# Kernel tuning notes

Measured on AMD Instinct MI355X. Metric: run time of the kernel, lower is better.

## Reference

```python
import jax, jax.numpy as jnp
import numpy as np

B, S, E = 2, 4096, 640
H, D, G = 4, 256, 1      # n_heads, head_dim, n_kv_groups
WINDOW = 512
SCALING = 256.0 ** -0.5  # query_pre_attn_scalar ** -0.5
EPS = 1e-6


def rmsnorm(x, scale):
    # Gemma variant: weight = 1 + scale, computed in fp32 over last dim
    xf = x.astype(jnp.float32)
    var = jnp.mean(xf * xf, axis=-1, keepdims=True)
    return (xf * jax.lax.rsqrt(var + EPS) * (1.0 + scale.astype(jnp.float32))).astype(x.dtype)


def apply_rope(x, cos, sin):
    # x: [B, h, S, D]; cos/sin: [S, D]
    half = x.shape[-1] // 2
    x1, x2 = x[..., :half], x[..., half:]
    rotated = jnp.concatenate([-x2, x1], axis=-1)
    return (x * cos[None, None] + rotated * sin[None, None]).astype(x.dtype)


def setup_inputs() -> dict:
    key = jax.random.key(0)
    ks = jax.random.split(key, 6)
    x = jax.random.normal(ks[0], (B, S, E), dtype=jnp.float32)
    # weights (torch Linear weight.T layout: [in, out])
    Wq = jax.random.normal(ks[1], (E, H * D), dtype=jnp.float32) * 0.02
    Wk = jax.random.normal(ks[2], (E, G * D), dtype=jnp.float32) * 0.02
    Wv = jax.random.normal(ks[3], (E, G * D), dtype=jnp.float32) * 0.02
    Wo = jax.random.normal(ks[4], (H * D, E), dtype=jnp.float32) * 0.02
    q_scale = jnp.zeros((D,), dtype=jnp.float32)
    k_scale = jnp.zeros((D,), dtype=jnp.float32)
    # RoPE tables (theta = rope_local_base = 10000 for sliding layers)
    inv_freq = 1.0 / (10000.0 ** (jnp.arange(0, D, 2, dtype=jnp.float32) / D))
    angles = jnp.arange(S, dtype=jnp.float32)[:, None] * inv_freq[None, :]
    angles = jnp.concatenate([angles, angles], axis=1)  # [S, D]
    cos, sin = jnp.cos(angles), jnp.sin(angles)
    # causal + sliding-window mask; True = masked out
    i = jnp.arange(S)[:, None]
    j = jnp.arange(S)[None, :]
    mask = (j > i) | ((i - j) >= WINDOW)
    return {"x": x, "mask": mask, "cos": cos, "sin": sin,
            "Wq": Wq, "Wk": Wk, "Wv": Wv, "Wo": Wo,
            "q_scale": q_scale, "k_scale": k_scale}


def reference(x, mask, cos, sin, Wq, Wk, Wv, Wo, q_scale, k_scale):
    b, s, _ = x.shape
    q = (x @ Wq).reshape(b, s, H, D).transpose(0, 2, 1, 3)  # [B,H,S,D]
    k = (x @ Wk).reshape(b, s, G, D).transpose(0, 2, 1, 3)  # [B,G,S,D]
    v = (x @ Wv).reshape(b, s, G, D).transpose(0, 2, 1, 3)  # [B,G,S,D]
    q = rmsnorm(q, q_scale)
    k = rmsnorm(k, k_scale)
    q = apply_rope(q, cos, sin)
    k = apply_rope(k, cos, sin)
    # GQA: K/V have G=1 heads; broadcasting replaces repeat_interleave
    scores = (q * SCALING) @ jnp.swapaxes(k, -1, -2)  # [B,H,S,S]
    scores = jnp.where(mask[None, None], -jnp.inf, scores)
    attn = jax.nn.softmax(scores, axis=-1)
    out = attn @ v                                     # [B,H,S,D]
    out = out.transpose(0, 2, 1, 3).reshape(b, s, H * D)
    return out @ Wo
```

## Files before the change

### kernel.cpp

```cpp
#include <hip/hip_runtime.h>
#include <hip/hip_bf16.h>
#include <stdint.h>

#define BB 2
#define SS 4096
#define EE 640
#define HH 4
#define DD 256
#define WIN 512

typedef __attribute__((ext_vector_type(8))) short bv8;
typedef __attribute__((ext_vector_type(4))) float fv4;
typedef __attribute__((ext_vector_type(16))) float fv16;

__device__ __forceinline__ unsigned short f2b(float f) {
  union { float f; unsigned u; } a; a.f = f;
  unsigned r = a.u + 0x7fffu + ((a.u >> 16) & 1u);
  return (unsigned short)(r >> 16);
}
__device__ __forceinline__ float b2f(unsigned short s) {
  union { unsigned u; float f; } a; a.u = ((unsigned)s) << 16;
  return a.f;
}
__device__ __forceinline__ unsigned pk2(float lo, float hi_) {
  return (unsigned)f2b(lo) | ((unsigned)f2b(hi_) << 16);
}

typedef const __attribute__((address_space(1))) unsigned int* as1u;
typedef __attribute__((address_space(3))) unsigned int* as3u;
__device__ __forceinline__ void gld16(const unsigned short* g, unsigned short* l) {
  __builtin_amdgcn_global_load_lds((as1u)(const void*)g, (as3u)(void*)l, 16, 0, 0);
}

__global__ __launch_bounds__(256) void k_cast_bf16(const float* __restrict__ src,
                                                   unsigned short* __restrict__ dst, int n4) {
  int i = blockIdx.x * 256 + threadIdx.x;
  if (i >= n4) return;
  fv4 v = ((const fv4*)src)[i];
  ushort4 o; o.x = f2b(v.x); o.y = f2b(v.y); o.z = f2b(v.z); o.w = f2b(v.w);
  ((ushort4*)dst)[i] = o;
}

__global__ __launch_bounds__(256) void k_wtrans(const float* __restrict__ Wq,
    const float* __restrict__ Wk, const float* __restrict__ Wv,
    const float* __restrict__ Wo, unsigned short* __restrict__ wqkv,
    unsigned short* __restrict__ wo) {
  __shared__ float tile[32][33];
  const int z = blockIdx.z, bx = blockIdx.x, by = blockIdx.y;
  const float* src; unsigned short* dst; int ss, ds;
  if (z == 0)      { if (bx >= 20 || by >= 32) return; src = Wq; dst = wqkv;              ss = 1024; ds = 640; }
  else if (z == 1) { if (bx >= 20 || by >= 8)  return; src = Wk; dst = wqkv + 1024 * 640; ss = 256;  ds = 640; }
  else if (z == 2) { if (bx >= 20 || by >= 8)  return; src = Wv; dst = wqkv + 1280 * 640; ss = 256;  ds = 640; }
  else             { if (bx >= 32 || by >= 20) return; src = Wo; dst = wo;                ss = 640;  ds = 1024; }
  int r0 = bx * 32, c0 = by * 32;
  int t = threadIdx.x;
  int rr = t >> 3, cc = (t & 7) * 4;
  fv4 x = *(const fv4*)(src + (size_t)(r0 + rr) * ss + c0 + cc);
#pragma unroll
  for (int i = 0; i < 4; ++i) tile[cc + i][rr] = x[i];
  __syncthreads();
  ushort4 o;
  o.x = f2b(tile[rr][cc + 0]); o.y = f2b(tile[rr][cc + 1]);
  o.z = f2b(tile[rr][cc + 2]); o.w = f2b(tile[rr][cc + 3]);
  *(ushort4*)(dst + (size_t)(c0 + rr) * ds + r0 + cc) = o;
}

__global__ __launch_bounds__(256) void k_gemm_qkv(const unsigned short* __restrict__ A,
    const unsigned short* __restrict__ Bt,
    const float* __restrict__ cosp, const float* __restrict__ sinp,
    const float* __restrict__ qsc, const float* __restrict__ ksc,
    unsigned short* __restrict__ qo, unsigned short* __restrict__ ko,
    unsigned short* __restrict__ vt) {
  __shared__ __align__(16) char shl[40960];
  unsigned short* la = (unsigned short*)shl;
  unsigned short* lb = (unsigned short*)(shl + 8192);
  const int K = EE;
  const int bid = blockIdx.x;
  const int gidx = (bid & 7) * 96 + (bid >> 3);
  const int mt = gidx / 6, nt = gidx % 6;
  const int m0 = mt * 64, n0 = nt * 256;
  const int tid = threadIdx.x, lane = tid & 63, wave = tid >> 6;
  const int g = lane >> 4, lr = lane & 15;
  const int wm = (wave >> 1) * 32, wn = (wave & 1) * 128;
  fv4 acc[2][8] = {};
  const unsigned short* ga0 = A + (size_t)(m0 + (tid >> 2)) * K + (tid & 3) * 8;
  const unsigned short* gb0 = Bt + (size_t)(n0 + (tid >> 2)) * K + (tid & 3) * 8;
  auto stage = [&](int k0, int pp) {
    gld16(ga0 + k0, la + pp * 2048 + wave * 512);
#pragma unroll
    for (int c = 0; c < 4; ++c)
      gld16(gb0 + (size_t)(c * 64) * K + k0, lb + pp * 8192 + (c * 64 + wave * 16) * 32);
  };
  stage(0, 0);
  const int NIT = K >> 5;
  for (int it = 0; it < NIT; ++it) {
    const int p = it & 1;
    if (it > 0) __builtin_amdgcn_s_barrier();
    if (it + 1 < NIT) {
      stage((it + 1) * 32, p ^ 1);
      asm volatile("s_waitcnt vmcnt(5)" ::: "memory");
    } else {
      asm volatile("s_waitcnt vmcnt(0)" ::: "memory");
    }
    __builtin_amdgcn_sched_barrier(0);
    __builtin_amdgcn_s_barrier();
    bv8 af[2], bf[8];
#pragma unroll
    for (int mi = 0; mi < 2; ++mi)
      af[mi] = *(const bv8*)(la + p * 2048 + (wm + mi * 16 + lr) * 32 + g * 8);
#pragma unroll
    for (int ni = 0; ni < 8; ++ni)
      bf[ni] = *(const bv8*)(lb + p * 8192 + (wn + ni * 16 + lr) * 32 + g * 8);
    __builtin_amdgcn_s_setprio(1);
#pragma unroll
    for (int mi = 0; mi < 2; ++mi)
#pragma unroll
      for (int ni = 0; ni < 8; ++ni)
        acc[mi][ni] = __builtin_amdgcn_mfma_f32_16x16x32_bf16(af[mi], bf[ni], acc[mi][ni], 0, 0, 0);
    __builtin_amdgcn_s_setprio(0);
  }
  __syncthreads();
  unsigned short* cw = (unsigned short*)shl;
  float* rsum = (float*)(shl + 33792);
#pragma unroll
  for (int mi = 0; mi < 2; ++mi)
#pragma unroll
    for (int r = 0; r < 4; ++r) {
      int row = wm + mi * 16 + g * 4 + r;
#pragma unroll
      for (int ni = 0; ni < 8; ++ni)
        cw[row * 264 + wn + ni * 16 + lr] = f2b(acc[mi][ni][r]);
    }
  __syncthreads();
  const int m = m0 + (tid & 63);
  const int b = m >> 12, s = m & 4095;
  if (nt < 5) {
    const int qq = tid >> 6;
    const int row = tid & 63;
    const int dlo = qq * 32, dhi = dlo + 128;
    float xlo[32], xhi[32];
    float ss2 = 0.f;
#pragma unroll
    for (int j8 = 0; j8 < 4; ++j8) {
      bv8 v0 = *(const bv8*)(cw + row * 264 + dlo + j8 * 8);
      bv8 v1 = *(const bv8*)(cw + row * 264 + dhi + j8 * 8);
#pragma unroll
      for (int e = 0; e < 8; ++e) {
        float a0 = b2f((unsigned short)v0[e]);
        float a1 = b2f((unsigned short)v1[e]);
        xlo[j8 * 8 + e] = a0; xhi[j8 * 8 + e] = a1;
        ss2 += a0 * a0 + a1 * a1;
      }
    }
    rsum[row * 4 + qq] = ss2;
    __syncthreads();
    float tot = rsum[row * 4 + 0] + rsum[row * 4 + 1] + rsum[row * 4 + 2] + rsum[row * 4 + 3];
    float rs = rsqrtf(tot * (1.0f / 256.0f) + 1e-6f);
    const float* scp = (nt < 4) ? qsc : ksc;
    const float mult = (nt < 4) ? (0.0625f * 1.44269504f) : 1.0f;
    unsigned short* dst = (nt < 4)
        ? qo + ((size_t)(b * HH + nt) * SS + s) * 256
        : ko + ((size_t)b * SS + s) * 256;
    const float* crow = cosp + (size_t)s * 256;
    const float* srow = sinp + (size_t)s * 256;
#pragma unroll
    for (int j4 = 0; j4 < 8; ++j4) {
      fv4 sclo = *(const fv4*)(scp + dlo + j4 * 4);
      fv4 schi = *(const fv4*)(scp + dhi + j4 * 4);
      fv4 clo = *(const fv4*)(crow + dlo + j4 * 4);
      fv4 chi = *(const fv4*)(crow + dhi + j4 * 4);
      fv4 slo = *(const fv4*)(srow + dlo + j4 * 4);
      fv4 shi = *(const fv4*)(srow + dhi + j4 * 4);
      ushort4 olo, ohi;
#pragma unroll
      for (int e = 0; e < 4; ++e) {
        float nlo = xlo[j4 * 4 + e] * rs * (1.0f + sclo[e]);
        float nhi = xhi[j4 * 4 + e] * rs * (1.0f + schi[e]);
        float rlo = (nlo * clo[e] - nhi * slo[e]) * mult;
        float rhi = (nhi * chi[e] + nlo * shi[e]) * mult;
        ((unsigned short*)&olo)[e] = f2b(rlo);
        ((unsigned short*)&ohi)[e] = f2b(rhi);
      }
      *(ushort4*)(dst + dlo + j4 * 4) = olo;
      *(ushort4*)(dst + dhi + j4 * 4) = ohi;
    }
  } else {
    const int d = tid;
    const int bb2 = (m0 >> 12), s0 = m0 & 4095;
    ushort4 buf[16];
#pragma unroll
    for (int r4 = 0; r4 < 16; ++r4) {
      ushort4 o;
      o.x = cw[(r4 * 4 + 0) * 264 + d];
      o.y = cw[(r4 * 4 + 1) * 264 + d];
      o.z = cw[(r4 * 4 + 2) * 264 + d];
      o.w = cw[(r4 * 4 + 3) * 264 + d];
      buf[r4] = o;
    }
    unsigned short* dst = vt + ((size_t)bb2 * 256 + d) * SS + s0;
#pragma unroll
    for (int r4 = 0; r4 < 16; ++r4) *(ushort4*)(dst + r4 * 4) = buf[r4];
  }
}

template <bool OUT_BF16, int BN>
__global__ __launch_bounds__(256) void k_gemm(const unsigned short* __restrict__ A,
    const unsigned short* __restrict__ Bt, void* __restrict__ Cp,
    int M, int N, int K, int nt_n) {
  __shared__ unsigned short la[2][128 * 32];
  __shared__ unsigned short lb[2][BN * 32];
  const int bid = blockIdx.x;
  const int gidx = (bid & 7) * (gridDim.x >> 3) + (bid >> 3);
  const int m0 = (gidx / nt_n) * 128, n0 = (gidx % nt_n) * BN;
  const int tid = threadIdx.x, lane = tid & 63, wave = tid >> 6;
  const int g = lane >> 4, lr = lane & 15;
  constexpr int MI = (BN == 128) ? 4 : 2;
  const int wm = (BN == 128) ? (wave >> 1) * 64 : wave * 32;
  const int wn = (BN == 128) ? (wave & 1) * 64 : 0;
  fv4 acc[MI][4] = {};
  const int srow = wave * 32 + (lane >> 2);
  const int sch = (lane & 3) * 8;
  const unsigned short* ga0 = A + (size_t)(m0 + srow) * K + sch;
  const int srowb = (BN == 128) ? srow : (wave * 16 + (lane >> 2));
  const unsigned short* gb0 = Bt + (size_t)(n0 + srowb) * K + sch;
  const int NIT = K >> 5;
  auto stage = [&](int k0, int pp) {
    unsigned short* lad = la[pp] + wave * 1024;
    unsigned short* lbd = lb[pp] + ((BN == 128) ? wave * 1024 : wave * 512);
    gld16(ga0 + k0, lad);
    gld16(ga0 + (size_t)16 * K + k0, lad + 512);
    gld16(gb0 + k0, lbd);
    if constexpr (BN == 128) gld16(gb0 + (size_t)16 * K + k0, lbd + 512);
  };
  stage(0, 0);
  for (int it = 0; it < NIT; ++it) {
    const int p = it & 1;
    if (it > 0) __builtin_amdgcn_s_barrier();
    if (it + 1 < NIT) {
      stage((it + 1) * 32, p ^ 1);
      if constexpr (BN == 128)
        asm volatile("s_waitcnt vmcnt(4)" ::: "memory");
      else
        asm volatile("s_waitcnt vmcnt(3)" ::: "memory");
    } else {
      asm volatile("s_waitcnt vmcnt(0)" ::: "memory");
    }
    __builtin_amdgcn_sched_barrier(0);
    __builtin_amdgcn_s_barrier();
    bv8 af[MI], bf[4];
#pragma unroll
    for (int mi = 0; mi < MI; ++mi)
      af[mi] = *(const bv8*)(la[p] + (wm + mi * 16 + lr) * 32 + g * 8);
#pragma unroll
    for (int ni = 0; ni < 4; ++ni)
      bf[ni] = *(const bv8*)(lb[p] + (wn + ni * 16 + lr) * 32 + g * 8);
    __builtin_amdgcn_s_setprio(1);
#pragma unroll
    for (int mi = 0; mi < MI; ++mi)
#pragma unroll
      for (int ni = 0; ni < 4; ++ni)
        acc[mi][ni] = __builtin_amdgcn_mfma_f32_16x16x32_bf16(af[mi], bf[ni], acc[mi][ni], 0, 0, 0);
    __builtin_amdgcn_s_setprio(0);
  }
#pragma unroll
  for (int mi = 0; mi < MI; ++mi) {
#pragma unroll
    for (int r = 0; r < 4; ++r) {
      size_t row = (size_t)(m0 + wm + mi * 16 + g * 4 + r);
#pragma unroll
      for (int ni = 0; ni < 4; ++ni) {
        int col = n0 + wn + ni * 16 + lr;
        float val = acc[mi][ni][r];
        if constexpr (OUT_BF16)
          ((unsigned short*)Cp)[row * N + col] = f2b(val);
        else
          ((float*)Cp)[row * N + col] = val;
      }
    }
  }
}

__global__ __launch_bounds__(512, 2) void k_attn(const unsigned short* __restrict__ q,
    const unsigned short* __restrict__ kg, const unsigned short* __restrict__ vtg,
    unsigned short* __restrict__ att) {
  __shared__ __align__(16) char ldsbuf[133120];
  __shared__ float lsb[4][32];
  unsigned short* kt = (unsigned short*)ldsbuf;
  unsigned short* vl = (unsigned short*)ldsbuf + 32768;
  const int bid = blockIdx.x;
  const int gidx = (bid & 7) * 32 + (bid >> 3);
  const int b = gidx >> 7;
  const int i0 = (gidx & 127) * 32;
  const int tid = threadIdx.x, wave = tid >> 6, lane = tid & 63;
  const int h = wave >> 1, ks = wave & 1;
  const int hi = lane >> 5, l31 = lane & 31;
  bv8 qf[16];
  {
    const unsigned short* qp = q + ((size_t)(b * HH + h) * SS + i0 + l31) * 256;
#pragma unroll
    for (int m = 0; m < 16; ++m) qf[m] = *(const bv8*)(qp + m * 16 + hi * 8);
  }
  fv16 po[8] = {};
  float lsp = 0.f;
  const int t0 = (i0 >= WIN) ? ((i0 - WIN + 1) >> 6) : 0;
  const int t1 = i0 >> 6;
  const unsigned short* kb = kg + (size_t)b * SS * 256;
  const unsigned short* vb = vtg + (size_t)b * 256 * SS;
  auto stageK = [&](int t, int pp) {
    const unsigned short* kbase = kb + (size_t)t * 64 * 256;
    unsigned short* dst = kt + pp * 16384;
#pragma unroll
    for (int c = 0; c < 4; ++c) {
      int slot = c * 512 + tid;
      int row = slot >> 5, s = slot & 31;
      gld16(kbase + (size_t)row * 256 + ((s ^ (row & 7)) * 8),
            dst + (c * 512 + wave * 64) * 8);
    }
  };
  auto stageV = [&](int t, int pp) {
    const unsigned short* vbase = vb + (size_t)t * 64;
    unsigned short* dst = vl + pp * 16384;
#pragma unroll
    for (int c = 0; c < 4; ++c) {
      int slot = c * 512 + tid;
      int d_ = slot >> 3, s = slot & 7;
      gld16(vbase + (size_t)d_ * SS + ((s ^ (d_ & 7)) * 8),
            dst + (c * 512 + wave * 64) * 8);
    }
  };
  stageK(t0, 0); stageV(t0, 0);
  int p = 0;
  const int krow = ks * 32 + l31;
  const int krx = krow & 7;
  const int vrx = l31 & 7;
  const float FSUB = 16.5f * 1.44269504f;
  for (int t = t0; t <= t1; ++t) {
    __syncthreads();
    if (t < t1) { stageK(t + 1, p ^ 1); stageV(t + 1, p ^ 1); }
    fv16 sa = {};
    const unsigned short* ktp = kt + p * 16384 + krow * 256;
    __builtin_amdgcn_s_setprio(1);
#pragma unroll
    for (int m = 0; m < 16; ++m) {
      bv8 kf = *(const bv8*)(ktp + (((m * 2 + hi) ^ krx) * 8));
      sa = __builtin_amdgcn_mfma_f32_32x32x16_bf16(kf, qf[m], sa, 0, 0, 0);
    }
    __builtin_amdgcn_s_setprio(0);
    const int kb0 = t * 64 + ks * 32;
    const bool nm = (kb0 + 31 > i0) || (i0 + 31 - kb0 >= WIN);
    if (nm) {
      const int qa = i0 + l31;
#pragma unroll
      for (int r = 0; r < 16; ++r) {
        int j = kb0 + (r & 3) + 8 * (r >> 2) + 4 * hi;
        if (j > qa || qa - j >= WIN) sa[r] = -1e30f;
      }
    }
    unsigned a[8];
#pragma unroll
    for (int i = 0; i < 8; ++i) {
      float e0 = exp2f(sa[2 * i] - FSUB);
      float e1 = exp2f(sa[2 * i + 1] - FSUB);
      lsp += e0 + e1;
      a[i] = pk2(e0, e1);
    }
    const unsigned short* vlp = vl + p * 16384;
    __builtin_amdgcn_s_setprio(1);
#pragma unroll
    for (int m2 = 0; m2 < 2; ++m2) {
      auto r02 = __builtin_amdgcn_permlane32_swap(a[m2 * 4 + 0], a[m2 * 4 + 2], false, false);
      auto r13 = __builtin_amdgcn_permlane32_swap(a[m2 * 4 + 1], a[m2 * 4 + 3], false, false);
      union { unsigned u[4]; bv8 v; } pf;
      pf.u[0] = r02[0]; pf.u[1] = r13[0]; pf.u[2] = r02[1]; pf.u[3] = r13[1];
      const int slot = (ks * 4 + m2 * 2 + hi) ^ vrx;
#pragma unroll
      for (int ds_ = 0; ds_ < 8; ++ds_) {
        bv8 vf = *(const bv8*)(vlp + (ds_ * 32 + l31) * 64 + slot * 8);
        po[ds_] = __builtin_amdgcn_mfma_f32_32x32x16_bf16(vf, pf.v, po[ds_], 0, 0, 0);
      }
    }
    __builtin_amdgcn_s_setprio(0);
    p ^= 1;
  }
  float lsfull = lsp + __shfl_xor(lsp, 32, 64);
  __syncthreads();
  float* cb = (float*)ldsbuf;
  if (ks == 1) {
#pragma unroll
    for (int ds_ = 0; ds_ < 8; ++ds_)
#pragma unroll
      for (int j = 0; j < 4; ++j) {
        int d0 = ds_ * 32 + 8 * j + 4 * hi;
        fv4 v4; v4[0] = po[ds_][4 * j]; v4[1] = po[ds_][4 * j + 1];
        v4[2] = po[ds_][4 * j + 2]; v4[3] = po[ds_][4 * j + 3];
        *(fv4*)(cb + (h * 32 + l31) * 260 + d0) = v4;
      }
    if (lane < 32) lsb[h][lane] = lsfull;
  }
  __syncthreads();
  if (ks == 0) {
    float total = lsfull + lsb[h][l31];
    float inv = 1.0f / total;
    unsigned short* op = att + ((size_t)b * SS + i0 + l31) * 1024 + h * 256;
#pragma unroll
    for (int ds_ = 0; ds_ < 8; ++ds_)
#pragma unroll
      for (int j = 0; j < 4; ++j) {
        int d0 = ds_ * 32 + 8 * j + 4 * hi;
        fv4 v4 = *(const fv4*)(cb + (h * 32 + l31) * 260 + d0);
        ushort4 o;
        o.x = f2b((po[ds_][4 * j] + v4[0]) * inv);
        o.y = f2b((po[ds_][4 * j + 1] + v4[1]) * inv);
        o.z = f2b((po[ds_][4 * j + 2] + v4[2]) * inv);
        o.w = f2b((po[ds_][4 * j + 3] + v4[3]) * inv);
        *(ushort4*)(op + d0) = o;
      }
  }
}

extern "C" void kernel_launch(void* const* d_in, const int* in_sizes, int n_in,
                              void* d_out, int out_size, void* d_ws, size_t ws_size,
                              hipStream_t stream) {
  const float* x    = (const float*)d_in[0];
  const float* cosp = (const float*)d_in[2];
  const float* sinp = (const float*)d_in[3];
  const float* Wq   = (const float*)d_in[4];
  const float* Wk   = (const float*)d_in[5];
  const float* Wv   = (const float*)d_in[6];
  const float* Wo   = (const float*)d_in[7];
  const float* qsc  = (const float*)d_in[8];
  const float* ksc  = (const float*)d_in[9];
  float* out = (float*)d_out;
  char* ws = (char*)d_ws;

  unsigned short* xb   = (unsigned short*)(ws);
  unsigned short* wqkv = (unsigned short*)(ws + 10485760);
  unsigned short* wo   = (unsigned short*)(ws + 12451840);
  unsigned short* qb   = (unsigned short*)(ws + 38928384);
  unsigned short* kbuf = (unsigned short*)(ws + 55705600);
  unsigned short* vt   = (unsigned short*)(ws + 59899904);
  unsigned short* attb = (unsigned short*)(ws + 64094208);

  k_cast_bf16<<<5120, 256, 0, stream>>>(x, xb, 1310720);
  k_wtrans<<<dim3(32, 32, 4), 256, 0, stream>>>(Wq, Wk, Wv, Wo, wqkv, wo);
  k_gemm_qkv<<<768, 256, 0, stream>>>(xb, wqkv, cosp, sinp, qsc, ksc, qb, kbuf, vt);
  k_attn<<<256, 512, 0, stream>>>(qb, kbuf, vt, attb);
  k_gemm<false, 64><<<640, 256, 0, stream>>>(attb, wo, out, 8192, 640, 1024, 10);
}
```

Measured before the change: 126.9 us.

## Apply RMSNorm and RoPE directly from MFMA registers in QKV GEMM epilogue

The QKV GEMM epilogue no longer stages the whole bf16 tile in LDS. It reduces the RMS sum of squares from accumulator registers with wave shuffles plus a small LDS exchange, then applies RoPE in registers. To make this work, the wave-to-column mapping is permuted so each lane holds matching lo/hi RoPE pairs. A cos/sin table in the matching layout is precomputed inside the weight-transpose kernel, and the V transpose now goes through a packed column-major LDS buffer with 16-byte stores. This removes an LDS round trip and the intermediate bf16 rounding before the norm, at the cost of scattered 2-byte global stores for Q/K.

```diff
diff --git a/kernel.cpp b/kernel.cpp
--- a/kernel.cpp
+++ b/kernel.cpp
@@ -43,17 +43,31 @@
 
 __global__ __launch_bounds__(256) void k_wtrans(const float* __restrict__ Wq,
     const float* __restrict__ Wk, const float* __restrict__ Wv,
-    const float* __restrict__ Wo, unsigned short* __restrict__ wqkv,
-    unsigned short* __restrict__ wo) {
+    const float* __restrict__ Wo, const float* __restrict__ cosp,
+    const float* __restrict__ sinp, unsigned short* __restrict__ wqkv,
+    unsigned short* __restrict__ wo, float* __restrict__ ctab) {
+  const int z = blockIdx.z, bx = blockIdx.x, by = blockIdx.y;
+  const int t = threadIdx.x;
+  if (z == 4) {
+    const int bb = bx * 32 + by;
+    const int s = bb * 4 + (t >> 6);
+#pragma unroll
+    for (int k = 0; k < 4; ++k) {
+      int c = (t & 63) * 4 + k;
+      int lr = c >> 4, wn2 = (c >> 3) & 1, j = c & 7;
+      int d = wn2 * 64 + (j & 3) * 16 + lr;
+      float v = (j < 4) ? cosp[(size_t)s * 256 + d] : sinp[(size_t)s * 256 + d];
+      ctab[(size_t)s * 256 + c] = v;
+    }
+    return;
+  }
   __shared__ float tile[32][33];
-  const int z = blockIdx.z, bx = blockIdx.x, by = blockIdx.y;
   const float* src; unsigned short* dst; int ss, ds;
   if (z == 0)      { if (bx >= 20 || by >= 32) return; src = Wq; dst = wqkv;              ss = 1024; ds = 640; }
   else if (z == 1) { if (bx >= 20 || by >= 8)  return; src = Wk; dst = wqkv + 1024 * 640; ss = 256;  ds = 640; }
   else if (z == 2) { if (bx >= 20 || by >= 8)  return; src = Wv; dst = wqkv + 1280 * 640; ss = 256;  ds = 640; }
   else             { if (bx >= 32 || by >= 20) return; src = Wo; dst = wo;                ss = 640;  ds = 1024; }
   int r0 = bx * 32, c0 = by * 32;
-  int t = threadIdx.x;
   int rr = t >> 3, cc = (t & 7) * 4;
   fv4 x = *(const fv4*)(src + (size_t)(r0 + rr) * ss + c0 + cc);
 #pragma unroll
@@ -66,8 +80,7 @@
 }
 
 __global__ __launch_bounds__(256) void k_gemm_qkv(const unsigned short* __restrict__ A,
-    const unsigned short* __restrict__ Bt,
-    const float* __restrict__ cosp, const float* __restrict__ sinp,
+    const unsigned short* __restrict__ Bt, const float* __restrict__ ctab,
     const float* __restrict__ qsc, const float* __restrict__ ksc,
     unsigned short* __restrict__ qo, unsigned short* __restrict__ ko,
     unsigned short* __restrict__ vt) {
@@ -81,7 +94,7 @@
   const int m0 = mt * 64, n0 = nt * 256;
   const int tid = threadIdx.x, lane = tid & 63, wave = tid >> 6;
   const int g = lane >> 4, lr = lane & 15;
-  const int wm = (wave >> 1) * 32, wn = (wave & 1) * 128;
+  const int wm = (wave >> 1) * 32, wn2 = wave & 1;
   fv4 acc[2][8] = {};
   const unsigned short* ga0 = A + (size_t)(m0 + (tid >> 2)) * K + (tid & 3) * 8;
   const unsigned short* gb0 = Bt + (size_t)(n0 + (tid >> 2)) * K + (tid & 3) * 8;
@@ -109,8 +122,10 @@
     for (int mi = 0; mi < 2; ++mi)
       af[mi] = *(const bv8*)(la + p * 2048 + (wm + mi * 16 + lr) * 32 + g * 8);
 #pragma unroll
-    for (int ni = 0; ni < 8; ++ni)
-      bf[ni] = *(const bv8*)(lb + p * 8192 + (wn + ni * 16 + lr) * 32 + g * 8);
+    for (int ni = 0; ni < 8; ++ni) {
+      int coln = wn2 * 64 + (ni & 3) * 16 + (ni >> 2) * 128 + lr;
+      bf[ni] = *(const bv8*)(lb + p * 8192 + coln * 32 + g * 8);
+    }
     __builtin_amdgcn_s_setprio(1);
 #pragma unroll
     for (int mi = 0; mi < 2; ++mi)
@@ -120,86 +135,87 @@
     __builtin_amdgcn_s_setprio(0);
   }
   __syncthreads();
-  unsigned short* cw = (unsigned short*)shl;
-  float* rsum = (float*)(shl + 33792);
-#pragma unroll
-  for (int mi = 0; mi < 2; ++mi)
-#pragma unroll
-    for (int r = 0; r < 4; ++r) {
-      int row = wm + mi * 16 + g * 4 + r;
-#pragma unroll
-      for (int ni = 0; ni < 8; ++ni)
-        cw[row * 264 + wn + ni * 16 + lr] = f2b(acc[mi][ni][r]);
-    }
-  __syncthreads();
-  const int m = m0 + (tid & 63);
-  const int b = m >> 12, s = m & 4095;
   if (nt < 5) {
-    const int qq = tid >> 6;
-    const int row = tid & 63;
-    const int dlo = qq * 32, dhi = dlo + 128;
-    float xlo[32], xhi[32];
-    float ss2 = 0.f;
-#pragma unroll
-    for (int j8 = 0; j8 < 4; ++j8) {
-      bv8 v0 = *(const bv8*)(cw + row * 264 + dlo + j8 * 8);
-      bv8 v1 = *(const bv8*)(cw + row * 264 + dhi + j8 * 8);
-#pragma unroll
-      for (int e = 0; e < 8; ++e) {
-        float a0 = b2f((unsigned short)v0[e]);
-        float a1 = b2f((unsigned short)v1[e]);
-        xlo[j8 * 8 + e] = a0; xhi[j8 * 8 + e] = a1;
-        ss2 += a0 * a0 + a1 * a1;
-      }
-    }
-    rsum[row * 4 + qq] = ss2;
+    float* rsum = (float*)(shl + 36864);
+    float part[2][4];
+#pragma unroll
+    for (int mi = 0; mi < 2; ++mi)
+#pragma unroll
+      for (int r = 0; r < 4; ++r) {
+        float ss2 = 0.f;
+#pragma unroll
+        for (int ni = 0; ni < 8; ++ni) ss2 += acc[mi][ni][r] * acc[mi][ni][r];
+        part[mi][r] = ss2;
+      }
+#pragma unroll
+    for (int off = 1; off < 16; off <<= 1)
+#pragma unroll
+      for (int mi = 0; mi < 2; ++mi)
+#pragma unroll
+        for (int r = 0; r < 4; ++r) part[mi][r] += __shfl_xor(part[mi][r], off, 64);
+    if (lr == 0) {
+#pragma unroll
+      for (int mi = 0; mi < 2; ++mi)
+#pragma unroll
+        for (int r = 0; r < 4; ++r)
+          rsum[(wm + mi * 16 + g * 4 + r) * 2 + wn2] = part[mi][r];
+    }
     __syncthreads();
-    float tot = rsum[row * 4 + 0] + rsum[row * 4 + 1] + rsum[row * 4 + 2] + rsum[row * 4 + 3];
-    float rs = rsqrtf(tot * (1.0f / 256.0f) + 1e-6f);
     const float* scp = (nt < 4) ? qsc : ksc;
     const float mult = (nt < 4) ? (0.0625f * 1.44269504f) : 1.0f;
-    unsigned short* dst = (nt < 4)
-        ? qo + ((size_t)(b * HH + nt) * SS + s) * 256
-        : ko + ((size_t)b * SS + s) * 256;
-    const float* crow = cosp + (size_t)s * 256;
-    const float* srow = sinp + (size_t)s * 256;
-#pragma unroll
-    for (int j4 = 0; j4 < 8; ++j4) {
-      fv4 sclo = *(const fv4*)(scp + dlo + j4 * 4);
-      fv4 schi = *(const fv4*)(scp + dhi + j4 * 4);
-      fv4 clo = *(const fv4*)(crow + dlo + j4 * 4);
-      fv4 chi = *(const fv4*)(crow + dhi + j4 * 4);
-      fv4 slo = *(const fv4*)(srow + dlo + j4 * 4);
-      fv4 shi = *(const fv4*)(srow + dhi + j4 * 4);
-      ushort4 olo, ohi;
-#pragma unroll
-      for (int e = 0; e < 4; ++e) {
-        float nlo = xlo[j4 * 4 + e] * rs * (1.0f + sclo[e]);
-        float nhi = xhi[j4 * 4 + e] * rs * (1.0f + schi[e]);
-        float rlo = (nlo * clo[e] - nhi * slo[e]) * mult;
-        float rhi = (nhi * chi[e] + nlo * shi[e]) * mult;
-        ((unsigned short*)&olo)[e] = f2b(rlo);
-        ((unsigned short*)&ohi)[e] = f2b(rhi);
-      }
-      *(ushort4*)(dst + dlo + j4 * 4) = olo;
-      *(ushort4*)(dst + dhi + j4 * 4) = ohi;
-    }
+    float scl[8];
+#pragma unroll
+    for (int ni = 0; ni < 8; ++ni) {
+      int d = wn2 * 64 + (ni & 3) * 16 + (ni >> 2) * 128 + lr;
+      scl[ni] = 1.0f + scp[d];
+    }
+#pragma unroll
+    for (int mi = 0; mi < 2; ++mi)
+#pragma unroll
+      for (int r = 0; r < 4; ++r) {
+        int row = wm + mi * 16 + g * 4 + r;
+        int mabs = m0 + row;
+        int bb = mabs >> 12, s = mabs & 4095;
+        float tot = rsum[row * 2 + 0] + rsum[row * 2 + 1];
+        float rs = rsqrtf(tot * (1.0f / 256.0f) + 1e-6f);
+        fv4 c4 = *(const fv4*)(ctab + (size_t)s * 256 + lr * 16 + wn2 * 8);
+        fv4 s4 = *(const fv4*)(ctab + (size_t)s * 256 + lr * 16 + wn2 * 8 + 4);
+        unsigned short* dst = (nt < 4)
+            ? qo + ((size_t)(bb * HH + nt) * SS + s) * 256
+            : ko + ((size_t)bb * SS + s) * 256;
+#pragma unroll
+        for (int j = 0; j < 4; ++j) {
+          float nlo = acc[mi][j][r] * rs * scl[j];
+          float nhi = acc[mi][j + 4][r] * rs * scl[j + 4];
+          float olo = (nlo * c4[j] - nhi * s4[j]) * mult;
+          float ohi = (nhi * c4[j] + nlo * s4[j]) * mult;
+          int dlo = wn2 * 64 + j * 16 + lr;
+          dst[dlo] = f2b(olo);
+          dst[dlo + 128] = f2b(ohi);
+        }
+      }
   } else {
+    unsigned short* vcol = (unsigned short*)shl;
+#pragma unroll
+    for (int mi = 0; mi < 2; ++mi)
+#pragma unroll
+      for (int ni = 0; ni < 8; ++ni) {
+        int col = wn2 * 64 + (ni & 3) * 16 + (ni >> 2) * 128 + lr;
+        int row0 = wm + mi * 16 + g * 4;
+        uint2 u;
+        u.x = pk2(acc[mi][ni][0], acc[mi][ni][1]);
+        u.y = pk2(acc[mi][ni][2], acc[mi][ni][3]);
+        *(uint2*)(vcol + col * 72 + row0) = u;
+      }
+    __syncthreads();
     const int d = tid;
-    const int bb2 = (m0 >> 12), s0 = m0 & 4095;
-    ushort4 buf[16];
-#pragma unroll
-    for (int r4 = 0; r4 < 16; ++r4) {
-      ushort4 o;
-      o.x = cw[(r4 * 4 + 0) * 264 + d];
-      o.y = cw[(r4 * 4 + 1) * 264 + d];
-      o.z = cw[(r4 * 4 + 2) * 264 + d];
-      o.w = cw[(r4 * 4 + 3) * 264 + d];
-      buf[r4] = o;
-    }
-    unsigned short* dst = vt + ((size_t)bb2 * 256 + d) * SS + s0;
-#pragma unroll
-    for (int r4 = 0; r4 < 16; ++r4) *(ushort4*)(dst + r4 * 4) = buf[r4];
+    const int bb0 = m0 >> 12, s0 = m0 & 4095;
+    unsigned short* dst = vt + ((size_t)bb0 * 256 + d) * SS + s0;
+#pragma unroll
+    for (int c8 = 0; c8 < 8; ++c8) {
+      bv8 v = *(const bv8*)(vcol + d * 72 + c8 * 8);
+      *(bv8*)(dst + c8 * 8) = v;
+    }
   }
 }
 
@@ -436,14 +452,15 @@
   unsigned short* xb   = (unsigned short*)(ws);
   unsigned short* wqkv = (unsigned short*)(ws + 10485760);
   unsigned short* wo   = (unsigned short*)(ws + 12451840);
+  float*          ctab = (float*)(ws + 13762560);
   unsigned short* qb   = (unsigned short*)(ws + 38928384);
   unsigned short* kbuf = (unsigned short*)(ws + 55705600);
   unsigned short* vt   = (unsigned short*)(ws + 59899904);
   unsigned short* attb = (unsigned short*)(ws + 64094208);
 
   k_cast_bf16<<<5120, 256, 0, stream>>>(x, xb, 1310720);
-  k_wtrans<<<dim3(32, 32, 4), 256, 0, stream>>>(Wq, Wk, Wv, Wo, wqkv, wo);
-  k_gemm_qkv<<<768, 256, 0, stream>>>(xb, wqkv, cosp, sinp, qsc, ksc, qb, kbuf, vt);
+  k_wtrans<<<dim3(32, 32, 5), 256, 0, stream>>>(Wq, Wk, Wv, Wo, cosp, sinp, wqkv, wo, ctab);
+  k_gemm_qkv<<<768, 256, 0, stream>>>(xb, wqkv, ctab, qsc, ksc, qb, kbuf, vt);
   k_attn<<<256, 512, 0, stream>>>(qb, kbuf, vt, attb);
   k_gemm<false, 64><<<640, 256, 0, stream>>>(attb, wo, out, 8192, 640, 1024, 10);
 }
```

Result: faster. 112.1 us (-11.7%).
